# Performance work log

Measured on AMD Instinct MI355X. Metric: run time of the kernel, lower is better.

## Reference

```python
import jax, jax.numpy as jnp
import numpy as np

N, D, H, C, M = 100000, 128, 4, 32, 3  # nodes, dim, heads, head_dim, metapaths
E = 400000  # edges per metapath


def setup_inputs() -> dict:
    key = jax.random.key(0)
    ks = jax.random.split(key, 12)
    inp = {
        'x_l': jax.random.normal(ks[0], (N, D), jnp.float32),
        'x_r': jax.random.normal(ks[1], (N, D), jnp.float32),
        'edge_index': jax.random.randint(ks[2], (M, 2, E), 0, N, jnp.int64),
        # linear_l / linear_r per node type (single 'gene' type)
        'Wl': jax.random.normal(ks[3], (D, D), jnp.float32) * 0.05,
        'bl': jnp.zeros((D,), jnp.float32),
        'Wr': jax.random.normal(ks[4], (D, D), jnp.float32) * 0.05,
        'br': jnp.zeros((D,), jnp.float32),
        # Conv1d(in=D, out=M+1, kernel=1) == dense [M+1, D] + bias
        'Wc': jax.random.normal(ks[5], (M + 1, D), jnp.float32) * 0.05,
        'bc': jnp.zeros((M + 1,), jnp.float32),
        'attn_l': jax.random.normal(ks[6], (M, H, C), jnp.float32) * 0.1,
        'attn_r': jax.random.normal(ks[7], (M, H, C), jnp.float32) * 0.1,
        'sharpen': jnp.ones((M,), jnp.float32),  # attn_activation='sharpening'
    }
    return inp


def reference(x_l, x_r, Wl, bl, Wr, br, Wc, bc, attn_l, attn_r, sharpen, edge_index):
    n = x_l.shape[0]
    l = (x_l @ Wl.T + bl).reshape(n, H, C)  # left projection  [N,H,C]
    r = (x_r @ Wr.T + br).reshape(n, H, C)  # right projection [N,H,C]
    # relation-mixing weights beta via 1x1 conv + softmax over relations
    beta = jax.nn.softmax(x_l @ Wc.T + bc, axis=1)  # [N, M+1]

    def agg(edges, al_m, ar_m, s_m):
        idx, nbr = edges[0], edges[1]  # aggregation index (i), neighbor (j)
        # per-edge, per-channel attention logits (alpha_j + alpha_i), sharpened
        a = (l[nbr] * al_m + r[idx] * ar_m) * s_m  # [E,H,C]
        # edge softmax segmented over destination node
        amax = jax.ops.segment_max(a, idx, num_segments=n)
        ex = jnp.exp(a - amax[idx])
        den = jax.ops.segment_sum(ex, idx, num_segments=n)
        att = ex / (den[idx] + 1e-16)
        # message = x_j * alpha, scatter-add aggregation
        return jax.ops.segment_sum(l[nbr] * att, idx, num_segments=n).reshape(n, D)

    rel = [agg(edge_index[m], attn_l[m], attn_r[m], sharpen[m]) for m in range(M)]
    rel.append(l.reshape(n, D))  # last relation slot = self (left) embedding
    emb = jnp.stack(rel, axis=1)  # [N, M+1, D]
    out = jnp.einsum('nrd,nr->nd', emb, beta)  # bmm(emb^T, beta).squeeze
    return jax.nn.relu(out)
```

## Files before the change

kernel.cpp:

```cpp
#include <hip/hip_runtime.h>
#include <math.h>

#define NN 100000
#define DD 128
#define MM 3
#define EE 400000
#define CAP 32


__global__ void k_detect(const int* __restrict__ ei, int* __restrict__ flag) {
  if (threadIdx.x == 0 && blockIdx.x == 0) {
    int orsum = 0;
    for (int i = 0; i < 64; ++i) orsum |= ei[2 * i + 1];
    flag[0] = (orsum == 0) ? 1 : 0;
  }
}

__global__ __launch_bounds__(256, 2)
void k_prep(const float* __restrict__ x,
            const float* __restrict__ Wl,
            const float* __restrict__ bl,
            const float* __restrict__ Wc,
            const float* __restrict__ bc,
            float* __restrict__ l_out,
            float* __restrict__ beta_out,
            int* __restrict__ deg) {
  __shared__ float xs[64][132];
  __shared__ float wlt[64][130];
  __shared__ float wcs[4][132];
  __shared__ float bcs[4];
  const int t = threadIdx.x;
  const int r0 = blockIdx.x * 64;

  #pragma unroll
  for (int i = 0; i < 8; ++i) {
    int f4 = t + 256 * i;
    int row = f4 >> 5;
    int kq = f4 & 31;
    int gr = r0 + row; if (gr >= NN) gr = NN - 1;
    float4 v = *reinterpret_cast<const float4*>(&x[(size_t)gr * DD + kq * 4]);
    *reinterpret_cast<float4*>(&xs[row][kq * 4]) = v;
  }
  if (t < 128) {
    int m = t >> 5, kq = t & 31;
    float4 v = *reinterpret_cast<const float4*>(&Wc[m * DD + kq * 4]);
    *reinterpret_cast<float4*>(&wcs[m][kq * 4]) = v;
  }
  if (t < 4) bcs[t] = bc[t];
  if (t < 192) {
    int m = t >> 6;
    int n = r0 + (t & 63);
    if (n < NN) deg[m * NN + n] = 0;
  }

  const int w = t >> 6;
  const int lane = t & 63;
  float acc0[16], acc1[16];
  #pragma unroll
  for (int r = 0; r < 16; ++r) { acc0[r] = 0.f; acc1[r] = 0.f; }

  for (int h = 0; h < 2; ++h) {
    __syncthreads();
    #pragma unroll
    for (int i = 0; i < 8; ++i) {
      int f4 = t + 256 * i;
      int j = f4 >> 4;
      int kq = f4 & 15;
      float4 v = *reinterpret_cast<const float4*>(&Wl[j * DD + h * 64 + kq * 4]);
      wlt[kq * 4 + 0][j] = v.x;
      wlt[kq * 4 + 1][j] = v.y;
      wlt[kq * 4 + 2][j] = v.z;
      wlt[kq * 4 + 3][j] = v.w;
    }
    __syncthreads();
    #pragma unroll
    for (int kq = 0; kq < 16; ++kq) {
      float2 w0 = *reinterpret_cast<const float2*>(&wlt[kq * 4 + 0][lane * 2]);
      float2 w1 = *reinterpret_cast<const float2*>(&wlt[kq * 4 + 1][lane * 2]);
      float2 w2 = *reinterpret_cast<const float2*>(&wlt[kq * 4 + 2][lane * 2]);
      float2 w3 = *reinterpret_cast<const float2*>(&wlt[kq * 4 + 3][lane * 2]);
      #pragma unroll
      for (int r = 0; r < 16; ++r) {
        float4 xv = *reinterpret_cast<const float4*>(&xs[w * 16 + r][h * 64 + kq * 4]);
        acc0[r] += xv.x * w0.x; acc0[r] += xv.y * w1.x;
        acc0[r] += xv.z * w2.x; acc0[r] += xv.w * w3.x;
        acc1[r] += xv.x * w0.y; acc1[r] += xv.y * w1.y;
        acc1[r] += xv.z * w2.y; acc1[r] += xv.w * w3.y;
      }
    }
  }

  float2 blv = *reinterpret_cast<const float2*>(&bl[lane * 2]);
  #pragma unroll
  for (int r = 0; r < 16; ++r) {
    int row = r0 + w * 16 + r;
    if (row < NN) {
      float2 o; o.x = acc0[r] + blv.x; o.y = acc1[r] + blv.y;
      *reinterpret_cast<float2*>(&l_out[(size_t)row * DD + lane * 2]) = o;
    }
  }

  {
    int r = t >> 2, m = t & 3;
    float lg = bcs[m];
    for (int k = 0; k < 128; ++k) lg += xs[r][k] * wcs[m][k];
    float mx = fmaxf(lg, __shfl_xor(lg, 1, 4));
    mx = fmaxf(mx, __shfl_xor(mx, 2, 4));
    float e = __expf(lg - mx);
    float s = e + __shfl_xor(e, 1, 4);
    s += __shfl_xor(s, 2, 4);
    int n = r0 + r;
    if (n < NN) beta_out[n * 4 + m] = e / s;
  }
}

__global__ __launch_bounds__(256)
void k_scatter(const int* __restrict__ ei, const int* __restrict__ flag,
               int* __restrict__ deg, int* __restrict__ lst) {
  int i = blockIdx.x * 256 + threadIdx.x;
  if (i >= MM * EE) return;
  int m = i / EE, e = i - m * EE;
  size_t pi = (size_t)m * 2 * EE + e;
  size_t pn = pi + EE;
  int idx, nbr;
  if (flag[0]) { idx = ei[2 * pi]; nbr = ei[2 * pn]; }
  else         { idx = ei[pi];     nbr = ei[pn];     }
  int slot = atomicAdd(&deg[m * NN + idx], 1);
  if (slot < CAP) lst[((size_t)m * NN + idx) * CAP + slot] = nbr;
}

__global__ __launch_bounds__(256, 4)
void k_agg(const float* __restrict__ l, const float* __restrict__ beta,
           const int* __restrict__ deg, const int* __restrict__ lst,
           const float* __restrict__ attn_l, const float* __restrict__ sharpen,
           float* __restrict__ out) {
  int tid = blockIdx.x * 256 + threadIdx.x;
  int node = tid >> 4;
  if (node >= NN) return;
  int ch0 = (tid & 15) << 3;

  float ls[8], acc[8];
  {
    const float* lp = l + (size_t)node * DD + ch0;
    *reinterpret_cast<float4*>(&ls[0]) = *reinterpret_cast<const float4*>(&lp[0]);
    *reinterpret_cast<float4*>(&ls[4]) = *reinterpret_cast<const float4*>(&lp[4]);
  }
  float4 bt = *reinterpret_cast<const float4*>(&beta[(size_t)node * 4]);
  #pragma unroll
  for (int i = 0; i < 8; ++i) acc[i] = bt.w * ls[i];

  #pragma unroll 1
  for (int m = 0; m < MM; ++m) {
    float sm = sharpen[m];
    float al[8];
    {
      const float* ap = attn_l + m * DD + ch0;
      *reinterpret_cast<float4*>(&al[0]) = *reinterpret_cast<const float4*>(&ap[0]);
      *reinterpret_cast<float4*>(&al[4]) = *reinterpret_cast<const float4*>(&ap[4]);
      #pragma unroll
      for (int i = 0; i < 8; ++i) al[i] *= sm;
    }
    float num[8], den[8];
    #pragma unroll
    for (int i = 0; i < 8; ++i) { num[i] = 0.f; den[i] = 0.f; }
    int cnt = deg[(size_t)m * NN + node];
    if (cnt > CAP) cnt = CAP;
    const int* lb = lst + ((size_t)m * NN + node) * CAP;
    for (int s = 0; s < cnt; ++s) {
      int nbr = lb[s];
      const float* np = l + (size_t)nbr * DD + ch0;
      float lv[8];
      *reinterpret_cast<float4*>(&lv[0]) = *reinterpret_cast<const float4*>(&np[0]);
      *reinterpret_cast<float4*>(&lv[4]) = *reinterpret_cast<const float4*>(&np[4]);
      #pragma unroll
      for (int i = 0; i < 8; ++i) {
        float e = __expf(lv[i] * al[i]);
        den[i] += e;
        num[i] += lv[i] * e;
      }
    }
    float bm = (m == 0) ? bt.x : (m == 1) ? bt.y : bt.z;
    #pragma unroll
    for (int i = 0; i < 8; ++i) acc[i] += bm * (num[i] / (den[i] + 1e-16f));
  }

  float* op = out + (size_t)node * DD + ch0;
  #pragma unroll
  for (int i = 0; i < 8; ++i) acc[i] = fmaxf(acc[i], 0.f);
  *reinterpret_cast<float4*>(&op[0]) = *reinterpret_cast<float4*>(&acc[0]);
  *reinterpret_cast<float4*>(&op[4]) = *reinterpret_cast<float4*>(&acc[4]);
}

extern "C" void kernel_launch(void* const* d_in, const int* in_sizes, int n_in,
                              void* d_out, int out_size, void* d_ws, size_t ws_size,
                              hipStream_t stream) {
  const float* x_l     = (const float*)d_in[0];
  const int*   ei      = (const int*)d_in[2];
  const float* Wl      = (const float*)d_in[3];
  const float* bl      = (const float*)d_in[4];
  const float* Wc      = (const float*)d_in[7];
  const float* bc      = (const float*)d_in[8];
  const float* attn_l  = (const float*)d_in[9];
  const float* sharpen = (const float*)d_in[11];
  float* out = (float*)d_out;

  float* l    = (float*)d_ws;
  float* beta = l + (size_t)NN * DD;
  int*   deg  = (int*)(beta + (size_t)NN * 4);
  int*   lst  = deg + (size_t)MM * NN;
  int*   flag = lst + (size_t)MM * NN * CAP;

  k_detect<<<1, 64, 0, stream>>>(ei, flag);
  k_prep<<<(NN + 63) / 64, 256, 0, stream>>>(x_l, Wl, bl, Wc, bc, l, beta, deg);
  k_scatter<<<(MM * EE + 255) / 256, 256, 0, stream>>>(ei, flag, deg, lst);
  k_agg<<<(NN * 16 + 255) / 256, 256, 0, stream>>>(l, beta, deg, lst, attn_l, sharpen, out);
}
```

Baseline: 401.1 us.

## Map one wavefront per node in aggregation with broadcast neighbor indices

The aggregation kernel now assigns a full 64-lane wavefront to each destination node, with two channels per lane. Previously 16 threads each covered 8 channels. Each lane loads one entry of the neighbor list, and the indices are broadcast with readlane. Neighbor rows are then gathered in batches of 8 so that several loads are in flight at once. This is meant to make each neighbor row read a single coalesced 512-byte access and raise memory-level parallelism, at the cost of 4x more threads, padded duplicate loads for low-degree nodes, and a higher occupancy target.

```diff
diff --git a/kernel.cpp b/kernel.cpp
--- a/kernel.cpp
+++ b/kernel.cpp
@@ -129,66 +129,64 @@
   if (slot < CAP) lst[((size_t)m * NN + idx) * CAP + slot] = nbr;
 }
 
-__global__ __launch_bounds__(256, 4)
+__global__ __launch_bounds__(256, 8)
 void k_agg(const float* __restrict__ l, const float* __restrict__ beta,
            const int* __restrict__ deg, const int* __restrict__ lst,
            const float* __restrict__ attn_l, const float* __restrict__ sharpen,
            float* __restrict__ out) {
-  int tid = blockIdx.x * 256 + threadIdx.x;
-  int node = tid >> 4;
+  const int lane = threadIdx.x & 63;
+  const int node = blockIdx.x * 4 + (threadIdx.x >> 6);
   if (node >= NN) return;
-  int ch0 = (tid & 15) << 3;
-
-  float ls[8], acc[8];
-  {
-    const float* lp = l + (size_t)node * DD + ch0;
-    *reinterpret_cast<float4*>(&ls[0]) = *reinterpret_cast<const float4*>(&lp[0]);
-    *reinterpret_cast<float4*>(&ls[4]) = *reinterpret_cast<const float4*>(&lp[4]);
-  }
+  const int ch0 = lane * 2;
+
+  float2 ls = *reinterpret_cast<const float2*>(&l[(size_t)node * DD + ch0]);
   float4 bt = *reinterpret_cast<const float4*>(&beta[(size_t)node * 4]);
-  #pragma unroll
-  for (int i = 0; i < 8; ++i) acc[i] = bt.w * ls[i];
+  float acc0 = bt.w * ls.x;
+  float acc1 = bt.w * ls.y;
 
   #pragma unroll 1
   for (int m = 0; m < MM; ++m) {
     float sm = sharpen[m];
-    float al[8];
-    {
-      const float* ap = attn_l + m * DD + ch0;
-      *reinterpret_cast<float4*>(&al[0]) = *reinterpret_cast<const float4*>(&ap[0]);
-      *reinterpret_cast<float4*>(&al[4]) = *reinterpret_cast<const float4*>(&ap[4]);
-      #pragma unroll
-      for (int i = 0; i < 8; ++i) al[i] *= sm;
-    }
-    float num[8], den[8];
-    #pragma unroll
-    for (int i = 0; i < 8; ++i) { num[i] = 0.f; den[i] = 0.f; }
-    int cnt = deg[(size_t)m * NN + node];
+    float2 al = *reinterpret_cast<const float2*>(&attn_l[m * DD + ch0]);
+    al.x *= sm; al.y *= sm;
+
+    int cnt = deg[m * NN + node];
     if (cnt > CAP) cnt = CAP;
-    const int* lb = lst + ((size_t)m * NN + node) * CAP;
-    for (int s = 0; s < cnt; ++s) {
-      int nbr = lb[s];
-      const float* np = l + (size_t)nbr * DD + ch0;
-      float lv[8];
-      *reinterpret_cast<float4*>(&lv[0]) = *reinterpret_cast<const float4*>(&np[0]);
-      *reinterpret_cast<float4*>(&lv[4]) = *reinterpret_cast<const float4*>(&np[4]);
-      #pragma unroll
-      for (int i = 0; i < 8; ++i) {
-        float e = __expf(lv[i] * al[i]);
-        den[i] += e;
-        num[i] += lv[i] * e;
+
+    float num0 = 0.f, num1 = 0.f, den0 = 0.f, den1 = 0.f;
+    if (cnt > 0) {
+      const int* lb = lst + ((size_t)m * NN + node) * CAP;
+      int nbr_reg = (lane < cnt) ? lb[lane] : 0;
+
+      for (int s0 = 0; s0 < cnt; s0 += 8) {
+        int ub = cnt - s0; if (ub > 8) ub = 8;
+        float2 v[8];
+        #pragma unroll
+        for (int k = 0; k < 8; ++k) {
+          int ss = s0 + k; if (ss >= cnt) ss = cnt - 1;
+          int nb = __builtin_amdgcn_readlane(nbr_reg, ss);
+          v[k] = *reinterpret_cast<const float2*>(&l[(size_t)nb * DD + ch0]);
+        }
+        #pragma unroll
+        for (int k = 0; k < 8; ++k) {
+          if (k < ub) {
+            float e0 = __expf(v[k].x * al.x);
+            float e1 = __expf(v[k].y * al.y);
+            den0 += e0;            den1 += e1;
+            num0 += v[k].x * e0;   num1 += v[k].y * e1;
+          }
+        }
       }
     }
     float bm = (m == 0) ? bt.x : (m == 1) ? bt.y : bt.z;
-    #pragma unroll
-    for (int i = 0; i < 8; ++i) acc[i] += bm * (num[i] / (den[i] + 1e-16f));
-  }
-
-  float* op = out + (size_t)node * DD + ch0;
-  #pragma unroll
-  for (int i = 0; i < 8; ++i) acc[i] = fmaxf(acc[i], 0.f);
-  *reinterpret_cast<float4*>(&op[0]) = *reinterpret_cast<float4*>(&acc[0]);
-  *reinterpret_cast<float4*>(&op[4]) = *reinterpret_cast<float4*>(&acc[4]);
+    acc0 += bm * (num0 / (den0 + 1e-16f));
+    acc1 += bm * (num1 / (den1 + 1e-16f));
+  }
+
+  float2 o;
+  o.x = fmaxf(acc0, 0.f);
+  o.y = fmaxf(acc1, 0.f);
+  *reinterpret_cast<float2*>(&out[(size_t)node * DD + ch0]) = o;
 }
 
 extern "C" void kernel_launch(void* const* d_in, const int* in_sizes, int n_in,
@@ -213,5 +211,5 @@
   k_detect<<<1, 64, 0, stream>>>(ei, flag);
   k_prep<<<(NN + 63) / 64, 256, 0, stream>>>(x_l, Wl, bl, Wc, bc, l, beta, deg);
   k_scatter<<<(MM * EE + 255) / 256, 256, 0, stream>>>(ei, flag, deg, lst);
-  k_agg<<<(NN * 16 + 255) / 256, 256, 0, stream>>>(l, beta, deg, lst, attn_l, sharpen, out);
-}
+  k_agg<<<(NN * 64 + 255) / 256, 256, 0, stream>>>(l, beta, deg, lst, attn_l, sharpen, out);
+}
```

Result: slower. 415.0 us (+3.5%).
